# Optimization experiments

Hardware: AMD Instinct MI355X
Metric: run time of the kernel (lower is better)

## Reference

```python
import jax, jax.numpy as jnp
import numpy as np

EPS_COS = 1e-8   # torch cosine_similarity eps
ATT_EPS = 1e-6   # LinearAttention eps
LN_EPS = 1e-5    # nn.LayerNorm default eps
NHEAD = 8
WS = 8           # window_size
TOPK = 16
C = 256          # embed_dim (hardcoded 256 in original gather)


def layer_norm(x, w, b):
    m = x.mean(-1, keepdims=True)
    v = ((x - m) ** 2).mean(-1, keepdims=True)
    return (x - m) / jnp.sqrt(v + LN_EPS) * w + b


def linear_attention(q, k, v):
    # q,k,v: [N, L, H, D]
    Q = jax.nn.elu(q) + 1.0
    K = jax.nn.elu(k) + 1.0
    L = v.shape[1]
    v = v / L
    KV = jnp.einsum('nshd,nshv->nhdv', K, v)
    Z = 1.0 / (jnp.einsum('nlhd,nhd->nlh', Q, K.sum(axis=1)) + ATT_EPS)
    return jnp.einsum('nlhd,nhdv,nlh->nlhv', Q, KV, Z) * L


def encoder_layer(x, source, Wq, Wk, Wv, Wm, W1, W2, n1w, n1b, n2w, n2b):
    bs, _, d = x.shape
    dim = d // NHEAD
    q = (x @ Wq).reshape(bs, -1, NHEAD, dim)
    k = (source @ Wk).reshape(bs, -1, NHEAD, dim)
    v = (source @ Wv).reshape(bs, -1, NHEAD, dim)
    msg = linear_attention(q, k, v).reshape(bs, -1, d) @ Wm
    msg = layer_norm(msg, n1w, n1b)
    msg = jax.nn.relu(jnp.concatenate([x, msg], axis=-1) @ W1) @ W2
    msg = layer_norm(msg, n2w, n2b)
    return x + msg


def topk_select(x, k):
    # x: [BN, S, C]; cosine similarity of each token to window mean, then topk
    avg = x.mean(axis=1, keepdims=True)                        # [BN,1,C]
    dot = (avg * x).sum(axis=-1)                               # [BN,S]
    na = jnp.maximum(jnp.linalg.norm(avg, axis=-1), EPS_COS)   # [BN,1]
    nb = jnp.maximum(jnp.linalg.norm(x, axis=-1), EPS_COS)     # [BN,S]
    cos = dot / (na * nb)
    _, idx = jax.lax.top_k(cos, k)                             # [BN,k]
    sel = jnp.take_along_axis(x, idx[:, :, None], axis=1)      # [BN,k,C]
    return sel, idx


def scatter_add(x, idx, src):
    # x: [BN,S,C], idx: [BN,k], src: [BN,k,C]
    BN, S, c = x.shape
    flat_idx = (jnp.arange(BN)[:, None] * S + idx).reshape(-1)
    return x.reshape(BN * S, c).at[flat_idx].add(src.reshape(-1, c)).reshape(BN, S, c)


def window_reverse_nchw(windows, ws, H, W):
    c = windows.shape[-1]
    x = windows.transpose(0, 2, 1).reshape(-1, H // ws, W // ws, c, ws, ws)
    return x.transpose(0, 3, 1, 4, 2, 5).reshape(-1, c, H, W)


def setup_inputs() -> dict:
    key = jax.random.key(0)
    ks = jax.random.split(key, 8)
    BN = 2 * 2304  # batch * nums_window
    s = 1.0 / np.sqrt(C)
    return {
        'x_win_attn': jax.random.normal(ks[0], (BN, WS * WS, C), jnp.float32),
        's_win_attn': jax.random.normal(ks[1], (BN, WS * WS, C), jnp.float32),
        'Wq': jax.random.normal(ks[2], (C, C), jnp.float32) * s,
        'Wk': jax.random.normal(ks[3], (C, C), jnp.float32) * s,
        'Wv': jax.random.normal(ks[4], (C, C), jnp.float32) * s,
        'Wmerge': jax.random.normal(ks[5], (C, C), jnp.float32) * s,
        'W1': jax.random.normal(ks[6], (2 * C, 2 * C), jnp.float32) * (1.0 / np.sqrt(2 * C)),
        'W2': jax.random.normal(ks[7], (2 * C, C), jnp.float32) * (1.0 / np.sqrt(2 * C)),
        'n1w': jnp.ones((C,), jnp.float32),
        'n1b': jnp.zeros((C,), jnp.float32),
        'n2w': jnp.ones((C,), jnp.float32),
        'n2b': jnp.zeros((C,), jnp.float32),
        'batch_size': 2,
        'nums_window': 2304,
        'h': 384,
        'w': 384,
    }


def reference(x_win_attn, s_win_attn, Wq, Wk, Wv, Wmerge, W1, W2,
              n1w, n1b, n2w, n2b, batch_size, nums_window, h, w):
    # 'cross' attention path of WinTopKAttention
    sel1, idx1 = topk_select(x_win_attn, TOPK)
    sel2, _ = topk_select(s_win_attn, TOPK)
    sel1 = sel1.reshape(batch_size, nums_window * TOPK, C)
    sel2 = sel2.reshape(batch_size, nums_window * TOPK, C)
    out = encoder_layer(sel1, sel2, Wq, Wk, Wv, Wmerge, W1, W2, n1w, n1b, n2w, n2b)
    out = out.reshape(batch_size * nums_window, TOPK, C)
    combined = scatter_add(x_win_attn, idx1, out)
    return window_reverse_nchw(combined, WS, h, w)
```

## Files before the change

kernel.cpp:

```cpp
#include <hip/hip_runtime.h>
#include <math.h>

static constexpr int BATCH = 2;
static constexpr int NWIN  = 2304;
static constexpr int BN    = BATCH * NWIN;
static constexpr int S     = 64;
static constexpr int CDIM  = 256;
static constexpr int TOPK_ = 16;
static constexpr int TROWS = BN * TOPK_;
static constexpr int LB    = NWIN * TOPK_;
static constexpr int HW    = 384;
static constexpr int KVSZ  = 8448;
static constexpr int KVB   = 384;
static constexpr int KVTOK = LB / KVB;

typedef unsigned short u16;
typedef unsigned long long u64;
typedef __attribute__((ext_vector_type(4))) float  f32x4;
typedef __attribute__((ext_vector_type(8))) short  bf16x8;

__device__ inline u16 f2bf(float f) {
    unsigned u = __float_as_uint(f);
    return (u16)((u + 0x7fffu + ((u >> 16) & 1u)) >> 16);
}
__device__ inline float bf2f(u16 b) {
    return __uint_as_float(((unsigned)b) << 16);
}

__device__ inline void load_lds16(const void* g, void* l) {
    __builtin_amdgcn_global_load_lds(
        (const __attribute__((address_space(1))) unsigned int*)g,
        (__attribute__((address_space(3))) unsigned int*)l, 16, 0, 0);
}

__global__ __launch_bounds__(256) void wconv_all_k(
    const float* __restrict__ Wq, const float* __restrict__ Wk,
    const float* __restrict__ Wv, const float* __restrict__ Wm,
    const float* __restrict__ W1, const float* __restrict__ W2,
    u16* __restrict__ Wqt, u16* __restrict__ Wkt, u16* __restrict__ Wvt,
    u16* __restrict__ Wmt, u16* __restrict__ W1t, u16* __restrict__ W2t)
{
    int t = blockIdx.x * 256 + threadIdx.x;
    const float* W; u16* Wt; int Nd, Kd;
    if (t < 262144) {
        const int sel = t >> 16; t &= 65535;
        W  = (sel == 0 ? Wq  : sel == 1 ? Wk  : sel == 2 ? Wv  : Wm);
        Wt = (sel == 0 ? Wqt : sel == 1 ? Wkt : sel == 2 ? Wvt : Wmt);
        Nd = 256; Kd = 256;
    } else if (t < 524288) { W = W1; Wt = W1t; Nd = 512; Kd = 512; t -= 262144; }
    else                   { W = W2; Wt = W2t; Nd = 256; Kd = 512; t -= 524288; }
    const int k = t / Nd, n = t - k * Nd;
    Wt[(size_t)n * Kd + k] = f2bf(W[t]);
}

__global__ __launch_bounds__(512) void topk_gather_k(
    const float* __restrict__ xin, const float* __restrict__ sin,
    u16* __restrict__ catp, u16* __restrict__ selS, int* __restrict__ idxX)
{
    __shared__ double2 pd[64 * 17];
    __shared__ double  avgd[256];
    __shared__ double  cosv[64];
    __shared__ int     rk[64];
    __shared__ int     slots[16];

    const int w    = blockIdx.x;
    const bool isX = (blockIdx.y == 0);
    const int tid  = threadIdx.x;
    const int cg   = tid & 63, rg = tid >> 6;
    const float* src = (isX ? xin : sin) + (size_t)w * S * CDIM;

    f32x4 v[8];
#pragma unroll
    for (int m = 0; m < 8; ++m)
        v[m] = *(const f32x4*)&src[(rg + 8 * m) * CDIM + cg * 4];

    double cs[4] = {0.0, 0.0, 0.0, 0.0};
#pragma unroll
    for (int m = 0; m < 8; ++m)
#pragma unroll
        for (int q = 0; q < 4; ++q)
            cs[q] += (double)v[m][q];

    double* red = (double*)pd;
#pragma unroll
    for (int q = 0; q < 4; ++q)
        red[rg * 256 + q * 64 + cg] = cs[q];
    __syncthreads();

    if (tid < 256) {
        const int qq = tid & 3, cc = tid >> 2;
        double sm = 0.0;
#pragma unroll
        for (int r = 0; r < 8; ++r) sm += red[r * 256 + qq * 64 + cc];
        avgd[tid] = sm * (1.0 / 64.0);
    }
    __syncthreads();

    {
        const double a0 = avgd[cg * 4 + 0], a1 = avgd[cg * 4 + 1];
        const double a2 = avgd[cg * 4 + 2], a3 = avgd[cg * 4 + 3];
        __syncthreads();
#pragma unroll
        for (int m = 0; m < 8; ++m) {
            const double x0 = (double)v[m][0], x1 = (double)v[m][1];
            const double x2 = (double)v[m][2], x3 = (double)v[m][3];
            double d = a0 * x0; d += a1 * x1; d += a2 * x2; d += a3 * x3;
            double n = x0 * x0; n += x1 * x1; n += x2 * x2; n += x3 * x3;
            d += __shfl_xor(d, 1); n += __shfl_xor(n, 1);
            d += __shfl_xor(d, 2); n += __shfl_xor(n, 2);
            if ((cg & 3) == 0)
                pd[(rg + 8 * m) * 17 + (cg >> 2)] = (double2){d, n};
        }
    }
    __syncthreads();

    {
        const int tok = tid >> 3, p = tid & 7;
        const double2 t0 = pd[tok * 17 + p * 2];
        const double2 t1 = pd[tok * 17 + p * 2 + 1];
        double sd = t0.x + t1.x, sn = t0.y + t1.y;
        sd += __shfl_xor(sd, 1); sd += __shfl_xor(sd, 2); sd += __shfl_xor(sd, 4);
        sn += __shfl_xor(sn, 1); sn += __shfl_xor(sn, 2); sn += __shfl_xor(sn, 4);
        if (p == 0) {
            double nb = sqrt(sn); if (nb < 1e-8) nb = 1e-8;
            cosv[tok] = sd / nb;
        }
    }
    __syncthreads();

    if (tid < 64) {
        const double ct = cosv[tid];
        int r = 0;
        for (int j = 0; j < 64; ++j) {
            const double cj = cosv[j];
            r += (cj > ct) || (cj == ct && j < tid);
        }
        rk[tid] = r;
        if (r < TOPK_) slots[r] = tid;
    }
    __syncthreads();

    if (isX && tid < TOPK_) idxX[w * TOPK_ + tid] = slots[tid];
#pragma unroll
    for (int m = 0; m < 8; ++m) {
        const int r = rg + 8 * m;
        const int j = rk[r];
        if (j < TOPK_) {
            u64 pk = (u64)f2bf(v[m][0]) | ((u64)f2bf(v[m][1]) << 16)
                   | ((u64)f2bf(v[m][2]) << 32) | ((u64)f2bf(v[m][3]) << 48);
            if (isX) *(u64*)&catp[((size_t)w * TOPK_ + j) * 512 + cg * 4] = pk;
            else     *(u64*)&selS[((size_t)w * TOPK_ + j) * 256 + cg * 4] = pk;
        }
    }
}

template<int EPI, int LNMODE>
__device__ inline void gemm_body8(
    const u16* __restrict__ A, int lda,
    const u16* __restrict__ Bt, int K,
    u16* __restrict__ Cout, int ldc,
    int m0, int n0,
    const float* __restrict__ gw, const float* __restrict__ gb,
    const float* __restrict__ xsrc, const int* __restrict__ idx)
{
    __shared__ u16 As[128 * 32];
    __shared__ u16 Bs[256 * 32];
    __shared__ float2 lnred[128][5];

    const int tid = threadIdx.x;
    const int lane = tid & 63, w = tid >> 6;
    const int wr = w >> 2, wc = w & 3;

    f32x4 acc[4][4];
#pragma unroll
    for (int i = 0; i < 4; ++i)
#pragma unroll
        for (int j = 0; j < 4; ++j)
            acc[i][j] = (f32x4){0.f, 0.f, 0.f, 0.f};

    const int rsel = lane & 15, ksel = (lane >> 4) * 8;

    for (int k0 = 0; k0 < K; k0 += 32) {
        {
            const int e = w * 512 + lane * 8;
            const int row = e >> 5, col = e & 31;
            load_lds16(&A[(size_t)(m0 + row) * lda + k0 + col], &As[w * 512]);
        }
#pragma unroll
        for (int i = 0; i < 2; ++i) {
            const int c = w + 8 * i;
            const int e = c * 512 + lane * 8;
            const int row = e >> 5, col = e & 31;
            load_lds16(&Bt[(size_t)(n0 + row) * K + k0 + col], &Bs[c * 512]);
        }
        __syncthreads();

        bf16x8 af[4], bfr[4];
#pragma unroll
        for (int i = 0; i < 4; ++i)
            af[i] = *(const bf16x8*)&As[(wr * 64 + i * 16 + rsel) * 32 + ksel];
#pragma unroll
        for (int j = 0; j < 4; ++j)
            bfr[j] = *(const bf16x8*)&Bs[(wc * 64 + j * 16 + rsel) * 32 + ksel];
#pragma unroll
        for (int i = 0; i < 4; ++i)
#pragma unroll
            for (int j = 0; j < 4; ++j)
                acc[i][j] = __builtin_amdgcn_mfma_f32_16x16x32_bf16(
                    af[i], bfr[j], acc[i][j], 0, 0, 0);
        __syncthreads();
    }

    const int g = lane >> 4, ccol = lane & 15;

    if (LNMODE == 0) {
#pragma unroll
        for (int i = 0; i < 4; ++i)
#pragma unroll
            for (int j = 0; j < 4; ++j)
#pragma unroll
                for (int r = 0; r < 4; ++r) {
                    float v = acc[i][j][r];
                    if (EPI == 1) v = (v > 0.f) ? (v + 1.f) : __expf(v);
                    if (EPI == 2) v = (v > 0.f) ? v : 0.f;
                    Cout[(size_t)(m0 + wr * 64 + i * 16 + g * 4 + r) * ldc
                         + (n0 + wc * 64 + j * 16 + ccol)] = f2bf(v);
                }
    } else {
#pragma unroll
        for (int i = 0; i < 4; ++i)
#pragma unroll
            for (int r = 0; r < 4; ++r) {
                float s = 0.f, q = 0.f;
#pragma unroll
                for (int j = 0; j < 4; ++j) {
                    const float v = acc[i][j][r];
                    s += v; q += v * v;
                }
#pragma unroll
                for (int m = 1; m < 16; m <<= 1) {
                    s += __shfl_xor(s, m); q += __shfl_xor(q, m);
                }
                if (ccol == 0)
                    lnred[wr * 64 + i * 16 + g * 4 + r][wc] = (float2){s, q};
            }
        __syncthreads();

#pragma unroll
        for (int i = 0; i < 4; ++i)
#pragma unroll
            for (int r = 0; r < 4; ++r) {
                const int lrow = wr * 64 + i * 16 + g * 4 + r;
                const float2 p0 = lnred[lrow][0], p1 = lnred[lrow][1];
                const float2 p2 = lnred[lrow][2], p3 = lnred[lrow][3];
                const float S = p0.x + p1.x + p2.x + p3.x;
                const float Q = p0.y + p1.y + p2.y + p3.y;
                const float mean = S * (1.f / 256.f);
                const float var  = Q * (1.f / 256.f) - mean * mean;
                const float rstd = rsqrtf(var + 1e-5f);
                const int row = m0 + lrow;
                const float* xr = nullptr;
                if (LNMODE == 2) {
                    const int tok = idx[row];
                    xr = xsrc + ((size_t)(row >> 4) * 64 + tok) * 256;
                }
#pragma unroll
                for (int j = 0; j < 4; ++j) {
                    const int col = wc * 64 + j * 16 + ccol;
                    float o = (acc[i][j][r] - mean) * rstd * gw[col] + gb[col];
                    if (LNMODE == 2) o += xr[col];
                    Cout[(size_t)row * ldc + col] = f2bf(o);
                }
            }
    }
}

template<int EPI, int LNMODE>
__global__ __launch_bounds__(512) void gemm8_k(
    const u16* __restrict__ A, int lda,
    const u16* __restrict__ Bt, int K,
    u16* __restrict__ Cout, int ldc,
    const float* __restrict__ gw, const float* __restrict__ gb,
    const float* __restrict__ xsrc, const int* __restrict__ idx)
{
    gemm_body8<EPI, LNMODE>(A, lda, Bt, K, Cout, ldc,
                            blockIdx.y * 128, blockIdx.x * 256,
                            gw, gb, xsrc, idx);
}

__global__ __launch_bounds__(512) void gemm_qkv_k(
    const u16* __restrict__ catA, const u16* __restrict__ selS,
    const u16* __restrict__ Wqt, const u16* __restrict__ Wkt,
    const u16* __restrict__ Wvt,
    u16* __restrict__ Qb, u16* __restrict__ Kb, u16* __restrict__ Vb)
{
    const int z = blockIdx.z;
    if (z == 0)
        gemm_body8<1, 0>(catA, 512, Wqt, 256, Qb, 256, blockIdx.y * 128, 0,
                         nullptr, nullptr, nullptr, nullptr);
    else if (z == 1)
        gemm_body8<1, 0>(selS, 256, Wkt, 256, Kb, 256, blockIdx.y * 128, 0,
                         nullptr, nullptr, nullptr, nullptr);
    else
        gemm_body8<0, 0>(selS, 256, Wvt, 256, Vb, 256, blockIdx.y * 128, 0,
                         nullptr, nullptr, nullptr, nullptr);
}

__global__ __launch_bounds__(256) void kv_part_k(
    const u16* __restrict__ Kb, const u16* __restrict__ Vb,
    float* __restrict__ part)
{
    __shared__ float Kt[16][256];
    __shared__ float Vt[16][256];

    const int bk = blockIdx.x;
    const int batch = bk / KVB, slot = bk % KVB;
    const size_t r0 = (size_t)batch * LB + (size_t)slot * KVTOK;
    const int h = threadIdx.x >> 5, e = threadIdx.x & 31;

    float acc[32] = {};
    float ks = 0.f;

    for (int tile = 0; tile < KVTOK / 16; ++tile) {
        const size_t rb = r0 + tile * 16;
        for (int i = 0; i < 16; ++i) {
            Kt[i][threadIdx.x] = bf2f(Kb[(rb + i) * 256 + threadIdx.x]);
            Vt[i][threadIdx.x] = bf2f(Vb[(rb + i) * 256 + threadIdx.x]);
        }
        __syncthreads();
        for (int s = 0; s < 16; ++s) {
            const float vv = Vt[s][(h << 5) + e];
            ks += Kt[s][(h << 5) + e];
#pragma unroll
            for (int d = 0; d < 32; ++d)
                acc[d] += Kt[s][(h << 5) + d] * vv;
        }
        __syncthreads();
    }

    float* pb = part + (size_t)bk * KVSZ;
    for (int d = 0; d < 32; ++d)
        pb[((h << 5) + d) * 32 + e] = acc[d];
    pb[8192 + threadIdx.x] = ks;
}

__global__ __launch_bounds__(256) void kv_reduce_k(
    const float* __restrict__ part, float* __restrict__ fin)
{
    __shared__ float r2[4][64];
    const int chunk = blockIdx.x;
    const int b = chunk / (KVSZ / 64);
    const int i0 = (chunk % (KVSZ / 64)) * 64;
    const int il = threadIdx.x & 63, pg = threadIdx.x >> 6;

    float s = 0.f;
    for (int p = pg; p < KVB; p += 4)
        s += part[(size_t)(b * KVB + p) * KVSZ + i0 + il];
    r2[pg][il] = s;
    __syncthreads();
    if (threadIdx.x < 64)
        fin[(size_t)b * KVSZ + i0 + threadIdx.x] =
            r2[0][threadIdx.x] + r2[1][threadIdx.x] +
            r2[2][threadIdx.x] + r2[3][threadIdx.x];
}

__global__ __launch_bounds__(256) void attn_apply_k(
    const u16* __restrict__ Q, const float* __restrict__ KV,
    u16* __restrict__ outp)
{
    __shared__ float kvs[8192];
    __shared__ float kss[256];
    __shared__ float qs[8][256];

    const int t0 = blockIdx.x * 64;
    const int batch = t0 / LB;
    const float* kvb = KV + (size_t)batch * KVSZ;
    for (int i = threadIdx.x; i < 8192; i += 256) kvs[i] = kvb[i];
    kss[threadIdx.x] = kvb[8192 + threadIdx.x];
    const int h = threadIdx.x >> 5, e = threadIdx.x & 31;
    __syncthreads();

    for (int o = 0; o < 64; o += 8) {
        __syncthreads();
        for (int i = 0; i < 8; ++i)
            qs[i][threadIdx.x] = bf2f(Q[(size_t)(t0 + o + i) * 256 + threadIdx.x]);
        __syncthreads();
        for (int tt = 0; tt < 8; ++tt) {
            const float* qh = &qs[tt][h << 5];
            float zq = 0.f, res = 0.f;
#pragma unroll
            for (int d = 0; d < 32; ++d) {
                const float qd = qh[d];
                zq  += qd * kss[(h << 5) + d];
                res += qd * kvs[((h << 5) + d) * 32 + e];
            }
            outp[(size_t)(t0 + o + tt) * 256 + threadIdx.x] = f2bf(res / (zq + 1e-6f));
        }
    }
}

__global__ __launch_bounds__(256) void combine_reverse_k(
    const float* __restrict__ xin, const int* __restrict__ idxX,
    const u16* __restrict__ outsel, float* __restrict__ outp)
{
    __shared__ float tile[128 * 33];
    __shared__ int   sidx[32];

    const int p  = blockIdx.x;
    const int c0 = blockIdx.y * 32;
    const int b  = p / 1152;
    const int rem = p % 1152;
    const int wy  = rem / 24, wxp = rem % 24;
    const int w0  = b * NWIN + wy * 48 + wxp * 2;
    const int tid = threadIdx.x;

    if (tid < 32) sidx[tid] = idxX[(w0 + (tid >> 4)) * TOPK_ + (tid & 15)];

    {
        const int r = tid >> 1, half = tid & 1;
        const int wl = r >> 6, t = r & 63;
        const float* srcp = xin + ((size_t)(w0 + wl) * 64 + t) * 256 + c0 + half * 16;
        const float4 v0 = ((const float4*)srcp)[0];
        const float4 v1 = ((const float4*)srcp)[1];
        const float4 v2 = ((const float4*)srcp)[2];
        const float4 v3 = ((const float4*)srcp)[3];
        float* dst = &tile[r * 33 + half * 16];
        dst[0] = v0.x; dst[1] = v0.y; dst[2]  = v0.z; dst[3]  = v0.w;
        dst[4] = v1.x; dst[5] = v1.y; dst[6]  = v1.z; dst[7]  = v1.w;
        dst[8] = v2.x; dst[9] = v2.y; dst[10] = v2.z; dst[11] = v2.w;
        dst[12] = v3.x; dst[13] = v3.y; dst[14] = v3.z; dst[15] = v3.w;
    }
    __syncthreads();

    for (int it = 0; it < 4; ++it) {
        const int rid = it * 8 + (tid >> 5);
        const int cc  = tid & 31;
        const int wl  = rid >> 4, j = rid & 15;
        const int t   = sidx[rid];
        tile[((wl << 6) + t) * 33 + cc] +=
            bf2f(outsel[((size_t)(w0 + wl) * TOPK_ + j) * 256 + c0 + cc]);
    }
    __syncthreads();

    const int chalf = tid >> 7;
    const int pix = tid & 127;
    const int dy = pix >> 4, x16 = pix & 15;
    const int wl = x16 >> 3, dx = x16 & 7;
    const int rr = (wl << 6) + dy * 8 + dx;
    const size_t obase = (((size_t)b * 256 + c0 + chalf) * HW + (wy * 8 + dy)) * HW
                       + wxp * 16 + x16;
    for (int cc = 0; cc < 32; cc += 2)
        outp[obase + (size_t)cc * (HW * HW)] = tile[rr * 33 + cc + chalf];
}

extern "C" void kernel_launch(void* const* d_in, const int* in_sizes, int n_in,
                              void* d_out, int out_size, void* d_ws, size_t ws_size,
                              hipStream_t stream)
{
    const float* x   = (const float*)d_in[0];
    const float* s   = (const float*)d_in[1];
    const float* Wq  = (const float*)d_in[2];
    const float* Wk  = (const float*)d_in[3];
    const float* Wv  = (const float*)d_in[4];
    const float* Wm  = (const float*)d_in[5];
    const float* W1  = (const float*)d_in[6];
    const float* W2  = (const float*)d_in[7];
    const float* n1w = (const float*)d_in[8];
    const float* n1b = (const float*)d_in[9];
    const float* n2w = (const float*)d_in[10];
    const float* n2b = (const float*)d_in[11];
    float* out = (float*)d_out;

    char* ws = (char*)d_ws;
    int*   idxX   = (int*)ws;
    float* KVpart = (float*)(ws + 294912);
    float* KVfin  = (float*)(ws + 26247168);
    u16*   Wqt    = (u16*)(ws + 26314752);
    u16*   Wkt    = (u16*)(ws + 26445824);
    u16*   Wvt    = (u16*)(ws + 26576896);
    u16*   Wmt    = (u16*)(ws + 26707968);
    u16*   W1t    = (u16*)(ws + 26839040);
    u16*   W2t    = (u16*)(ws + 27363328);
    u16*   Qb     = (u16*)(ws + 27625472);
    u16*   Kb     = (u16*)(ws + 65374208);
    u16*   Vb     = (u16*)(ws + 103122944);
    u16*   osel   = (u16*)(ws + 140871680);

    u16* catA  = (u16*)d_out;
    u16* selSb = (u16*)((char*)d_out + 75497472);
    u16* msgA  = (u16*)((char*)d_out + 113246208);
    u16* Hb    = (u16*)((char*)d_out + 150994944);

    wconv_all_k<<<dim3(2560), 256, 0, stream>>>(Wq, Wk, Wv, Wm, W1, W2,
                                                Wqt, Wkt, Wvt, Wmt, W1t, W2t);

    topk_gather_k<<<dim3(BN, 2), 512, 0, stream>>>(x, s, catA, selSb, idxX);

    gemm_qkv_k<<<dim3(1, 576, 3), 512, 0, stream>>>(catA, selSb, Wqt, Wkt, Wvt,
                                                    Qb, Kb, Vb);

    kv_part_k<<<dim3(2 * KVB), 256, 0, stream>>>(Kb, Vb, KVpart);
    kv_reduce_k<<<dim3(2 * (KVSZ / 64)), 256, 0, stream>>>(KVpart, KVfin);

    attn_apply_k<<<dim3(TROWS / 64), 256, 0, stream>>>(Qb, KVfin, msgA);

    gemm8_k<0, 1><<<dim3(1, 576), 512, 0, stream>>>(
        msgA, 256, Wmt, 256, catA + 256, 512, n1w, n1b, nullptr, nullptr);

    gemm8_k<2, 0><<<dim3(2, 576), 512, 0, stream>>>(
        catA, 512, W1t, 512, Hb, 512, nullptr, nullptr, nullptr, nullptr);

    gemm8_k<0, 2><<<dim3(1, 576), 512, 0, stream>>>(
        Hb, 512, W2t, 512, osel, 256, n2w, n2b, x, idxX);

    combine_reverse_k<<<dim3(BN / 2, 8), 256, 0, stream>>>(x, idxX, osel, out);
}
```

Before: 682.7 us.

## Fuse attention apply into merge GEMM with LayerNorm; smaller tiles for W2 GEMM

Linear-attention output for each head is now computed per 64-row tile straight into shared memory and fed to the Wm MFMA GEMM with LayerNorm1 in the epilogue. This removes the msgA round trip through global memory and one kernel launch. The W2+LN2 GEMM moves to a dedicated kernel with 64-row tiles and 256 threads, doubling the block count for occupancy. The top-k rank computation is spread across all 512 threads with shuffle reductions instead of 64 serial threads. The fused kernel uses a large LDS footprint of about 50KB, which may limit occupancy, and it recomputes per-head scalar attention work inside each block.

```diff
diff --git a/kernel.cpp b/kernel.cpp
--- a/kernel.cpp
+++ b/kernel.cpp
@@ -128,15 +128,21 @@
     }
     __syncthreads();
 
-    if (tid < 64) {
-        const double ct = cosv[tid];
+    {
+        const int t = tid >> 3, p = tid & 7;
+        const double ct = cosv[t];
         int r = 0;
-        for (int j = 0; j < 64; ++j) {
+#pragma unroll
+        for (int i = 0; i < 8; ++i) {
+            const int j = p * 8 + i;
             const double cj = cosv[j];
-            r += (cj > ct) || (cj == ct && j < tid);
-        }
-        rk[tid] = r;
-        if (r < TOPK_) slots[r] = tid;
+            r += (cj > ct) || (cj == ct && j < t);
+        }
+        r += __shfl_xor(r, 1); r += __shfl_xor(r, 2); r += __shfl_xor(r, 4);
+        if (p == 0) {
+            rk[t] = r;
+            if (r < TOPK_) slots[r] = t;
+        }
     }
     __syncthreads();
 
@@ -154,18 +160,15 @@
     }
 }
 
-template<int EPI, int LNMODE>
+template<int EPI>
 __device__ inline void gemm_body8(
     const u16* __restrict__ A, int lda,
     const u16* __restrict__ Bt, int K,
     u16* __restrict__ Cout, int ldc,
-    int m0, int n0,
-    const float* __restrict__ gw, const float* __restrict__ gb,
-    const float* __restrict__ xsrc, const int* __restrict__ idx)
+    int m0, int n0)
 {
     __shared__ u16 As[128 * 32];
     __shared__ u16 Bs[256 * 32];
-    __shared__ float2 lnred[128][5];
 
     const int tid = threadIdx.x;
     const int lane = tid & 63, w = tid >> 6;
@@ -212,80 +215,27 @@
     }
 
     const int g = lane >> 4, ccol = lane & 15;
-
-    if (LNMODE == 0) {
-#pragma unroll
-        for (int i = 0; i < 4; ++i)
-#pragma unroll
-            for (int j = 0; j < 4; ++j)
-#pragma unroll
-                for (int r = 0; r < 4; ++r) {
-                    float v = acc[i][j][r];
-                    if (EPI == 1) v = (v > 0.f) ? (v + 1.f) : __expf(v);
-                    if (EPI == 2) v = (v > 0.f) ? v : 0.f;
-                    Cout[(size_t)(m0 + wr * 64 + i * 16 + g * 4 + r) * ldc
-                         + (n0 + wc * 64 + j * 16 + ccol)] = f2bf(v);
-                }
-    } else {
-#pragma unroll
-        for (int i = 0; i < 4; ++i)
+#pragma unroll
+    for (int i = 0; i < 4; ++i)
+#pragma unroll
+        for (int j = 0; j < 4; ++j)
 #pragma unroll
             for (int r = 0; r < 4; ++r) {
-                float s = 0.f, q = 0.f;
-#pragma unroll
-                for (int j = 0; j < 4; ++j) {
-                    const float v = acc[i][j][r];
-                    s += v; q += v * v;
-                }
-#pragma unroll
-                for (int m = 1; m < 16; m <<= 1) {
-                    s += __shfl_xor(s, m); q += __shfl_xor(q, m);
-                }
-                if (ccol == 0)
-                    lnred[wr * 64 + i * 16 + g * 4 + r][wc] = (float2){s, q};
-            }
-        __syncthreads();
-
-#pragma unroll
-        for (int i = 0; i < 4; ++i)
-#pragma unroll
-            for (int r = 0; r < 4; ++r) {
-                const int lrow = wr * 64 + i * 16 + g * 4 + r;
-                const float2 p0 = lnred[lrow][0], p1 = lnred[lrow][1];
-                const float2 p2 = lnred[lrow][2], p3 = lnred[lrow][3];
-                const float S = p0.x + p1.x + p2.x + p3.x;
-                const float Q = p0.y + p1.y + p2.y + p3.y;
-                const float mean = S * (1.f / 256.f);
-                const float var  = Q * (1.f / 256.f) - mean * mean;
-                const float rstd = rsqrtf(var + 1e-5f);
-                const int row = m0 + lrow;
-                const float* xr = nullptr;
-                if (LNMODE == 2) {
-                    const int tok = idx[row];
-                    xr = xsrc + ((size_t)(row >> 4) * 64 + tok) * 256;
-                }
-#pragma unroll
-                for (int j = 0; j < 4; ++j) {
-                    const int col = wc * 64 + j * 16 + ccol;
-                    float o = (acc[i][j][r] - mean) * rstd * gw[col] + gb[col];
-                    if (LNMODE == 2) o += xr[col];
-                    Cout[(size_t)row * ldc + col] = f2bf(o);
-                }
-            }
-    }
-}
-
-template<int EPI, int LNMODE>
+                float v = acc[i][j][r];
+                if (EPI == 1) v = (v > 0.f) ? (v + 1.f) : __expf(v);
+                if (EPI == 2) v = (v > 0.f) ? v : 0.f;
+                Cout[(size_t)(m0 + wr * 64 + i * 16 + g * 4 + r) * ldc
+                     + (n0 + wc * 64 + j * 16 + ccol)] = f2bf(v);
+            }
+}
+
+template<int EPI>
 __global__ __launch_bounds__(512) void gemm8_k(
     const u16* __restrict__ A, int lda,
     const u16* __restrict__ Bt, int K,
-    u16* __restrict__ Cout, int ldc,
-    const float* __restrict__ gw, const float* __restrict__ gb,
-    const float* __restrict__ xsrc, const int* __restrict__ idx)
-{
-    gemm_body8<EPI, LNMODE>(A, lda, Bt, K, Cout, ldc,
-                            blockIdx.y * 128, blockIdx.x * 256,
-                            gw, gb, xsrc, idx);
+    u16* __restrict__ Cout, int ldc)
+{
+    gemm_body8<EPI>(A, lda, Bt, K, Cout, ldc, blockIdx.y * 128, blockIdx.x * 256);
 }
 
 __global__ __launch_bounds__(512) void gemm_qkv_k(
@@ -296,14 +246,11 @@
 {
     const int z = blockIdx.z;
     if (z == 0)
-        gemm_body8<1, 0>(catA, 512, Wqt, 256, Qb, 256, blockIdx.y * 128, 0,
-                         nullptr, nullptr, nullptr, nullptr);
+        gemm_body8<1>(catA, 512, Wqt, 256, Qb, 256, blockIdx.y * 128, 0);
     else if (z == 1)
-        gemm_body8<1, 0>(selS, 256, Wkt, 256, Kb, 256, blockIdx.y * 128, 0,
-                         nullptr, nullptr, nullptr, nullptr);
+        gemm_body8<1>(selS, 256, Wkt, 256, Kb, 256, blockIdx.y * 128, 0);
     else
-        gemm_body8<0, 0>(selS, 256, Wvt, 256, Vb, 256, blockIdx.y * 128, 0,
-                         nullptr, nullptr, nullptr, nullptr);
+        gemm_body8<0>(selS, 256, Wvt, 256, Vb, 256, blockIdx.y * 128, 0);
 }
 
 __global__ __launch_bounds__(256) void kv_part_k(
@@ -364,39 +311,224 @@
             r2[2][threadIdx.x] + r2[3][threadIdx.x];
 }
 
-__global__ __launch_bounds__(256) void attn_apply_k(
-    const u16* __restrict__ Q, const float* __restrict__ KV,
-    u16* __restrict__ outp)
-{
+__global__ __launch_bounds__(256) void attn_merge_ln_k(
+    const u16* __restrict__ Qb, const float* __restrict__ KVfin,
+    const u16* __restrict__ Wmt, u16* __restrict__ Cout,
+    const float* __restrict__ gw, const float* __restrict__ gb)
+{
+    __shared__ u16   As[64 * 32];
+    __shared__ u16   Bs[256 * 32];
+    __shared__ u16   Qs[64 * 36];
     __shared__ float kvs[8192];
     __shared__ float kss[256];
-    __shared__ float qs[8][256];
-
-    const int t0 = blockIdx.x * 64;
-    const int batch = t0 / LB;
-    const float* kvb = KV + (size_t)batch * KVSZ;
-    for (int i = threadIdx.x; i < 8192; i += 256) kvs[i] = kvb[i];
-    kss[threadIdx.x] = kvb[8192 + threadIdx.x];
-    const int h = threadIdx.x >> 5, e = threadIdx.x & 31;
-    __syncthreads();
-
-    for (int o = 0; o < 64; o += 8) {
-        __syncthreads();
-        for (int i = 0; i < 8; ++i)
-            qs[i][threadIdx.x] = bf2f(Q[(size_t)(t0 + o + i) * 256 + threadIdx.x]);
-        __syncthreads();
-        for (int tt = 0; tt < 8; ++tt) {
-            const float* qh = &qs[tt][h << 5];
-            float zq = 0.f, res = 0.f;
-#pragma unroll
-            for (int d = 0; d < 32; ++d) {
-                const float qd = qh[d];
-                zq  += qd * kss[(h << 5) + d];
-                res += qd * kvs[((h << 5) + d) * 32 + e];
-            }
-            outp[(size_t)(t0 + o + tt) * 256 + threadIdx.x] = f2bf(res / (zq + 1e-6f));
-        }
-    }
+    __shared__ float2 lnred[64][5];
+
+    const int tid = threadIdx.x;
+    const int lane = tid & 63, w = tid >> 6;
+    const int m0 = blockIdx.x * 64;
+    const int batch = m0 / LB;
+    const float* kvb = KVfin + (size_t)batch * KVSZ;
+
+    for (int i = tid; i < 8192; i += 256) kvs[i] = kvb[i];
+    kss[tid] = kvb[8192 + tid];
+
+    f32x4 acc[4][4];
+#pragma unroll
+    for (int i = 0; i < 4; ++i)
+#pragma unroll
+        for (int j = 0; j < 4; ++j)
+            acc[i][j] = (f32x4){0.f, 0.f, 0.f, 0.f};
+
+    const int rsel = lane & 15, ksel = (lane >> 4) * 8;
+    const int qrow = tid >> 2, qsub = tid & 3;
+    const int ecol = tid & 31, tg = tid >> 5;
+
+    for (int h = 0; h < 8; ++h) {
+        *(bf16x8*)&Qs[qrow * 36 + qsub * 8] =
+            *(const bf16x8*)&Qb[(size_t)(m0 + qrow) * 256 + h * 32 + qsub * 8];
+#pragma unroll
+        for (int i = 0; i < 4; ++i) {
+            const int c = w + 4 * i;
+            const int e = c * 512 + lane * 8;
+            const int row = e >> 5, col = e & 31;
+            load_lds16(&Wmt[(size_t)row * 256 + h * 32 + col], &Bs[c * 512]);
+        }
+        __syncthreads();
+
+        {
+            float res[8] = {}, zq[8] = {};
+#pragma unroll
+            for (int dc = 0; dc < 4; ++dc) {
+                float kv8[8], ks8[8];
+#pragma unroll
+                for (int di = 0; di < 8; ++di) {
+                    kv8[di] = kvs[(h * 32 + dc * 8 + di) * 32 + ecol];
+                    ks8[di] = kss[h * 32 + dc * 8 + di];
+                }
+#pragma unroll
+                for (int m = 0; m < 8; ++m) {
+                    const bf16x8 qv = *(const bf16x8*)&Qs[(tg * 8 + m) * 36 + dc * 8];
+#pragma unroll
+                    for (int di = 0; di < 8; ++di) {
+                        const float q = bf2f((u16)qv[di]);
+                        zq[m]  += q * ks8[di];
+                        res[m] += q * kv8[di];
+                    }
+                }
+            }
+#pragma unroll
+            for (int m = 0; m < 8; ++m)
+                As[(tg * 8 + m) * 32 + ecol] = f2bf(res[m] / (zq[m] + 1e-6f));
+        }
+        __syncthreads();
+
+        bf16x8 af[4], bfr[4];
+#pragma unroll
+        for (int i = 0; i < 4; ++i)
+            af[i] = *(const bf16x8*)&As[(i * 16 + rsel) * 32 + ksel];
+#pragma unroll
+        for (int j = 0; j < 4; ++j)
+            bfr[j] = *(const bf16x8*)&Bs[(w * 64 + j * 16 + rsel) * 32 + ksel];
+#pragma unroll
+        for (int i = 0; i < 4; ++i)
+#pragma unroll
+            for (int j = 0; j < 4; ++j)
+                acc[i][j] = __builtin_amdgcn_mfma_f32_16x16x32_bf16(
+                    af[i], bfr[j], acc[i][j], 0, 0, 0);
+        __syncthreads();
+    }
+
+    const int g = lane >> 4, ccol = lane & 15;
+#pragma unroll
+    for (int i = 0; i < 4; ++i)
+#pragma unroll
+        for (int r = 0; r < 4; ++r) {
+            float s = 0.f, q = 0.f;
+#pragma unroll
+            for (int j = 0; j < 4; ++j) {
+                const float v = acc[i][j][r];
+                s += v; q += v * v;
+            }
+#pragma unroll
+            for (int m = 1; m < 16; m <<= 1) {
+                s += __shfl_xor(s, m); q += __shfl_xor(q, m);
+            }
+            if (ccol == 0) lnred[i * 16 + g * 4 + r][w] = (float2){s, q};
+        }
+    __syncthreads();
+#pragma unroll
+    for (int i = 0; i < 4; ++i)
+#pragma unroll
+        for (int r = 0; r < 4; ++r) {
+            const int lrow = i * 16 + g * 4 + r;
+            const float2 p0 = lnred[lrow][0], p1 = lnred[lrow][1];
+            const float2 p2 = lnred[lrow][2], p3 = lnred[lrow][3];
+            const float Sm = p0.x + p1.x + p2.x + p3.x;
+            const float Qm = p0.y + p1.y + p2.y + p3.y;
+            const float mean = Sm * (1.f / 256.f);
+            const float rstd = rsqrtf(Qm * (1.f / 256.f) - mean * mean + 1e-5f);
+#pragma unroll
+            for (int j = 0; j < 4; ++j) {
+                const int col = w * 64 + j * 16 + ccol;
+                Cout[(size_t)(m0 + lrow) * 512 + col] =
+                    f2bf((acc[i][j][r] - mean) * rstd * gw[col] + gb[col]);
+            }
+        }
+}
+
+__global__ __launch_bounds__(256) void gemm_w2_ln2_k(
+    const u16* __restrict__ A, const u16* __restrict__ Bt,
+    u16* __restrict__ Cout,
+    const float* __restrict__ gw, const float* __restrict__ gb,
+    const float* __restrict__ xsrc, const int* __restrict__ idx)
+{
+    __shared__ u16 As[64 * 32];
+    __shared__ u16 Bs[256 * 32];
+    __shared__ float2 lnred[64][5];
+
+    const int tid = threadIdx.x;
+    const int lane = tid & 63, w = tid >> 6;
+    const int m0 = blockIdx.x * 64;
+
+    f32x4 acc[4][4];
+#pragma unroll
+    for (int i = 0; i < 4; ++i)
+#pragma unroll
+        for (int j = 0; j < 4; ++j)
+            acc[i][j] = (f32x4){0.f, 0.f, 0.f, 0.f};
+
+    const int rsel = lane & 15, ksel = (lane >> 4) * 8;
+
+    for (int k0 = 0; k0 < 512; k0 += 32) {
+        {
+            const int e = w * 512 + lane * 8;
+            const int row = e >> 5, col = e & 31;
+            load_lds16(&A[(size_t)(m0 + row) * 512 + k0 + col], &As[w * 512]);
+        }
+#pragma unroll
+        for (int i = 0; i < 4; ++i) {
+            const int c = w + 4 * i;
+            const int e = c * 512 + lane * 8;
+            const int row = e >> 5, col = e & 31;
+            load_lds16(&Bt[(size_t)row * 512 + k0 + col], &Bs[c * 512]);
+        }
+        __syncthreads();
+
+        bf16x8 af[4], bfr[4];
+#pragma unroll
+        for (int i = 0; i < 4; ++i)
+            af[i] = *(const bf16x8*)&As[(i * 16 + rsel) * 32 + ksel];
+#pragma unroll
+        for (int j = 0; j < 4; ++j)
+            bfr[j] = *(const bf16x8*)&Bs[(w * 64 + j * 16 + rsel) * 32 + ksel];
+#pragma unroll
+        for (int i = 0; i < 4; ++i)
+#pragma unroll
+            for (int j = 0; j < 4; ++j)
+                acc[i][j] = __builtin_amdgcn_mfma_f32_16x16x32_bf16(
+                    af[i], bfr[j], acc[i][j], 0, 0, 0);
+        __syncthreads();
+    }
+
+    const int g = lane >> 4, ccol = lane & 15;
+#pragma unroll
+    for (int i = 0; i < 4; ++i)
+#pragma unroll
+        for (int r = 0; r < 4; ++r) {
+            float s = 0.f, q = 0.f;
+#pragma unroll
+            for (int j = 0; j < 4; ++j) {
+                const float v = acc[i][j][r];
+                s += v; q += v * v;
+            }
+#pragma unroll
+            for (int m = 1; m < 16; m <<= 1) {
+                s += __shfl_xor(s, m); q += __shfl_xor(q, m);
+            }
+            if (ccol == 0) lnred[i * 16 + g * 4 + r][w] = (float2){s, q};
+        }
+    __syncthreads();
+#pragma unroll
+    for (int i = 0; i < 4; ++i)
+#pragma unroll
+        for (int r = 0; r < 4; ++r) {
+            const int lrow = i * 16 + g * 4 + r;
+            const float2 p0 = lnred[lrow][0], p1 = lnred[lrow][1];
+            const float2 p2 = lnred[lrow][2], p3 = lnred[lrow][3];
+            const float Sm = p0.x + p1.x + p2.x + p3.x;
+            const float Qm = p0.y + p1.y + p2.y + p3.y;
+            const float mean = Sm * (1.f / 256.f);
+            const float rstd = rsqrtf(Qm * (1.f / 256.f) - mean * mean + 1e-5f);
+            const int row = m0 + lrow;
+            const float* xr = xsrc + ((size_t)(row >> 4) * 64 + idx[row]) * 256;
+#pragma unroll
+            for (int j = 0; j < 4; ++j) {
+                const int col = w * 64 + j * 16 + ccol;
+                const float o = (acc[i][j][r] - mean) * rstd * gw[col] + gb[col]
+                              + xr[col];
+                Cout[(size_t)row * 256 + col] = f2bf(o);
+            }
+        }
 }
 
 __global__ __launch_bounds__(256) void combine_reverse_k(
@@ -488,7 +620,6 @@
 
     u16* catA  = (u16*)d_out;
     u16* selSb = (u16*)((char*)d_out + 75497472);
-    u16* msgA  = (u16*)((char*)d_out + 113246208);
     u16* Hb    = (u16*)((char*)d_out + 150994944);
 
     wconv_all_k<<<dim3(2560), 256, 0, stream>>>(Wq, Wk, Wv, Wm, W1, W2,
@@ -502,16 +633,13 @@
     kv_part_k<<<dim3(2 * KVB), 256, 0, stream>>>(Kb, Vb, KVpart);
     kv_reduce_k<<<dim3(2 * (KVSZ / 64)), 256, 0, stream>>>(KVpart, KVfin);
 
-    attn_apply_k<<<dim3(TROWS / 64), 256, 0, stream>>>(Qb, KVfin, msgA);
-
-    gemm8_k<0, 1><<<dim3(1, 576), 512, 0, stream>>>(
-        msgA, 256, Wmt, 256, catA + 256, 512, n1w, n1b, nullptr, nullptr);
-
-    gemm8_k<2, 0><<<dim3(2, 576), 512, 0, stream>>>(
-        catA, 512, W1t, 512, Hb, 512, nullptr, nullptr, nullptr, nullptr);
-
-    gemm8_k<0, 2><<<dim3(1, 576), 512, 0, stream>>>(
-        Hb, 512, W2t, 512, osel, 256, n2w, n2b, x, idxX);
+    attn_merge_ln_k<<<dim3(TROWS / 64), 256, 0, stream>>>(
+        Qb, KVfin, Wmt, catA + 256, n1w, n1b);
+
+    gemm8_k<2><<<dim3(2, 576), 512, 0, stream>>>(catA, 512, W1t, 512, Hb, 512);
+
+    gemm_w2_ln2_k<<<dim3(TROWS / 64), 256, 0, stream>>>(
+        Hb, W2t, osel, n2w, n2b, x, idxX);
 
     combine_reverse_k<<<dim3(BN / 2, 8), 256, 0, stream>>>(x, idxX, osel, out);
 }
```

Measured after the change: 726.5 us. +6.4%, slower.
